# Kernel optimization log

Hardware: AMD Instinct MI355X
Metric: run time of the kernel (lower is better)

Reference implementation:

```python
import jax, jax.numpy as jnp
import numpy as np

EMB, HID, SEQ, BATCH, VOCAB, NLAYERS = 512, 512, 64, 64, 10000, 2


def setup_inputs() -> dict:
    key = jax.random.key(0)
    ks = jax.random.split(key, 8)
    u = lambda k, s: jax.random.uniform(k, s, jnp.float32, -0.1, 0.1)
    return {
        "inputs": jax.random.randint(ks[0], (SEQ, BATCH), 0, VOCAB),  # (S,B) token ids
        "hidden": jnp.zeros((NLAYERS, BATCH, HID), jnp.float32),      # init_hidden()
        "emb": u(ks[1], (VOCAB, EMB)),                                # embedding table
        "W0": u(ks[2], (HID, EMB)),  "bW0": jnp.zeros((HID,), jnp.float32),
        "W1": u(ks[3], (HID, HID)), "bW1": jnp.zeros((HID,), jnp.float32),
        "U0": u(ks[4], (HID, HID)), "bU0": jnp.zeros((HID,), jnp.float32),
        "U1": u(ks[5], (HID, HID)), "bU1": jnp.zeros((HID,), jnp.float32),
        "Wd": u(ks[6], (VOCAB, HID)), "bd": jnp.zeros((VOCAB,), jnp.float32),
    }


def reference(inputs, hidden, emb, W0, bW0, W1, bW1, U0, bU0, U1, bU1, Wd, bd):
    # Stacked 2-layer Elman RNN; dp_keep_prob=1.0 -> dropout is identity.
    x = emb[inputs]  # (S,B,E) embedding lookup for all timesteps at once

    def step(h, x_t):
        # h: (2,B,H); x_t: (B,E)
        h0 = jnp.tanh(x_t @ W0.T + bW0 + h[0] @ U0.T + bU0)   # layer 0
        h1 = jnp.tanh(h0 @ W1.T + bW1 + h[1] @ U1.T + bU1)    # layer 1
        logits = h1 @ Wd.T + bd                                # (B,V)
        return jnp.stack([h0, h1]), logits

    h_final, logits = jax.lax.scan(step, hidden, x)
    return logits, h_final  # (S,B,V), (2,B,H)
```

## Files before the change

### kernel.cpp

```cpp
#include <hip/hip_runtime.h>
#include <hip/hip_bf16.h>
#include <hip/hip_fp16.h>


typedef _Float16 f16;
typedef _Float16 f16x8 __attribute__((ext_vector_type(8)));
typedef float fvec4 __attribute__((ext_vector_type(4)));
typedef float f32x4 __attribute__((ext_vector_type(4)));
typedef unsigned int u32;
typedef u32 u32x2 __attribute__((ext_vector_type(2)));

__device__ __forceinline__ f32x4 mfma16(f16x8 a, f16x8 b, f32x4 c) {
    return __builtin_amdgcn_mfma_f32_16x16x32_f16(a, b, c, 0, 0, 0);
}

__device__ __forceinline__ f16x8 cvt_f16x8(fvec4 a, fvec4 b) {
    f16x8 r;
    r[0] = (f16)a[0]; r[1] = (f16)a[1]; r[2] = (f16)a[2]; r[3] = (f16)a[3];
    r[4] = (f16)b[0]; r[5] = (f16)b[1]; r[6] = (f16)b[2]; r[7] = (f16)b[3];
    return r;
}

__global__ void cvt_f32_f16(const float* __restrict__ src, f16* __restrict__ dst, int n8) {
    int i = blockIdx.x * 256 + threadIdx.x;
    if (i >= n8) return;
    const fvec4* p = (const fvec4*)(src + (size_t)i * 8);
    *(f16x8*)(dst + (size_t)i * 8) = cvt_f16x8(p[0], p[1]);
}

__global__ void cvt_wd(const float* __restrict__ src, f16* __restrict__ dst) {
    int i = blockIdx.x * 256 + threadIdx.x;
    if (i >= 647168) return;
    if (i < 640000) {
        const fvec4* p = (const fvec4*)(src + (size_t)i * 8);
        *(f16x8*)(dst + (size_t)i * 8) = cvt_f16x8(p[0], p[1]);
    } else {
        f16x8 z = {};
        *(f16x8*)(dst + (size_t)i * 8) = z;
    }
}

__global__ void gather_x(const int* __restrict__ toks, const float* __restrict__ emb,
                         f16* __restrict__ xb) {
    int i = blockIdx.x * 256 + threadIdx.x;
    if (i >= 262144) return;
    int row = i >> 6, seg = i & 63;
    int tok = toks[row];
    const fvec4* p = (const fvec4*)(emb + (size_t)tok * 512 + seg * 8);
    *(f16x8*)(xb + (size_t)row * 512 + seg * 8) = cvt_f16x8(p[0], p[1]);
}

template <int MODE>
__global__ __launch_bounds__(256) void gemm_bt(
    const f16* __restrict__ A, const f16* __restrict__ Bm,
    const float* __restrict__ bias1, const float* __restrict__ bias2,
    float* __restrict__ C, int N)
{
    const int tM = blockIdx.x * 128;
    const int tN = blockIdx.y * 128;
    const int tid = threadIdx.x;
    const int l = tid & 63, w = tid >> 6;
    const int wr = w >> 1, wc = w & 1;
    const int l15 = l & 15, l4 = l >> 4;

    __shared__ f16 As[128 * 40];
    __shared__ f16 Bs[128 * 40];

    f32x4 acc[4][4] = {};

    for (int ks = 0; ks < 16; ++ks) {
        const int k0 = ks * 32;
        __syncthreads();
#pragma unroll
        for (int it = 0; it < 2; ++it) {
            int c = tid + it * 256;
            int row = c >> 2, seg = c & 3;
            *(f16x8*)(&As[row * 40 + seg * 8]) =
                *(const f16x8*)(A + (size_t)(tM + row) * 512 + k0 + seg * 8);
            *(f16x8*)(&Bs[row * 40 + seg * 8]) =
                *(const f16x8*)(Bm + (size_t)(tN + row) * 512 + k0 + seg * 8);
        }
        __syncthreads();
        f16x8 af[4], bf[4];
#pragma unroll
        for (int m = 0; m < 4; ++m)
            af[m] = *(const f16x8*)(&As[(wr * 64 + m * 16 + l15) * 40 + 8 * l4]);
#pragma unroll
        for (int n = 0; n < 4; ++n)
            bf[n] = *(const f16x8*)(&Bs[(wc * 64 + n * 16 + l15) * 40 + 8 * l4]);
#pragma unroll
        for (int m = 0; m < 4; ++m)
#pragma unroll
            for (int n = 0; n < 4; ++n)
                acc[m][n] = mfma16(af[m], bf[n], acc[m][n]);
    }

    if (MODE == 0) {
#pragma unroll
        for (int n = 0; n < 4; ++n) {
            int col = tN + wc * 64 + n * 16 + l15;
            if (col >= N) continue;
            float bsum = (bias1 ? bias1[col] : 0.f) + (bias2 ? bias2[col] : 0.f);
#pragma unroll
            for (int m = 0; m < 4; ++m)
#pragma unroll
                for (int r = 0; r < 4; ++r) {
                    int row = tM + wr * 64 + m * 16 + l4 * 4 + r;
                    C[(size_t)row * N + col] = acc[m][n][r] + bsum;
                }
        }
    } else {
        const int t  = blockIdx.x * 2 + wr;
        const int wp = blockIdx.y * 2 + wc;
        const int lp_hi = (l15 >> 2) * 16;
        const int rp = l15 & 3;
#pragma unroll
        for (int n = 0; n < 4; ++n) {
            int col = tN + wc * 64 + n * 16 + l15;
            float bsum = bias1[col] + bias2[col];
#pragma unroll
            for (int m = 0; m < 4; ++m) {
#pragma unroll
                for (int r = 0; r < 4; ++r) {
                    int lanep = lp_hi + l4 * 4 + r;
                    size_t idx = ((((size_t)t * 4 + m) * 8 + wp) * 64 + lanep) * 16
                                 + n * 4 + rp;
                    C[idx] = acc[m][n][r] + bsum;
                }
            }
        }
    }
}

__global__ __launch_bounds__(512, 1) void recur_kernel(
    const float* __restrict__ A0p,
    const float* __restrict__ U,
    const float* __restrict__ h0,
    f16* __restrict__ Hh,
    float* __restrict__ outTail)
{
    const int g = blockIdx.x;
    const int tid = threadIdx.x;
    const int l = tid & 63, w = tid >> 6;
    const int l15 = l & 15, l4 = l >> 4;
    const int colbase = w * 64;

    __shared__ __align__(16) char smem[163840];
    char* hsb  = smem;
    char* ldsB = smem + 32768;

    f16x8 bf[4][12];
#pragma unroll
    for (int nt = 0; nt < 4; ++nt) {
        const float* urow = U + (size_t)(colbase + nt * 16 + l15) * 512 + 8 * l4;
#pragma unroll
        for (int kk = 0; kk < 12; ++kk) {
            const fvec4* p = (const fvec4*)(urow + kk * 32);
            bf[nt][kk] = cvt_f16x8(p[0], p[1]);
        }
#pragma unroll
        for (int kk = 12; kk < 16; ++kk) {
            const fvec4* p = (const fvec4*)(urow + kk * 32);
            *(f16x8*)(ldsB + ((w * 4 + nt) * 4 + (kk - 12)) * 1024 + l * 16) =
                cvt_f16x8(p[0], p[1]);
        }
    }
    for (int c = tid; c < 1024; c += 512) {
        int row = c >> 6, seg = c & 63;
        const fvec4* p = (const fvec4*)(h0 + (size_t)(g * 16 + row) * 512 + seg * 8);
        *(f16x8*)(hsb + row * 1024 + ((seg * 16) ^ ((row & 7) << 4))) =
            cvt_f16x8(p[0], p[1]);
    }
    __syncthreads();

    const int sw = (l15 & 7) << 4;
    const int rowbase = l15 * 1024;

    for (int t = 0; t < 64; ++t) {
        const float* ab = A0p + (((size_t)t * 4 + g) * 8 + w) * 1024 + l * 16;
        f32x4 acc[4];
#pragma unroll
        for (int nt = 0; nt < 4; ++nt) acc[nt] = *(const fvec4*)(ab + nt * 4);

        const char* hrd = hsb + (t & 1) * 16384 + rowbase;
#pragma unroll
        for (int kk = 0; kk < 12; ++kk) {
            f16x8 h = *(const f16x8*)(hrd + ((kk * 64 + l4 * 16) ^ sw));
            acc[0] = mfma16(bf[0][kk], h, acc[0]);
            acc[1] = mfma16(bf[1][kk], h, acc[1]);
            acc[2] = mfma16(bf[2][kk], h, acc[2]);
            acc[3] = mfma16(bf[3][kk], h, acc[3]);
        }
#pragma unroll
        for (int kk = 12; kk < 16; ++kk) {
            f16x8 h = *(const f16x8*)(hrd + ((kk * 64 + l4 * 16) ^ sw));
#pragma unroll
            for (int nt = 0; nt < 4; ++nt) {
                f16x8 u = *(const f16x8*)(ldsB + ((w * 4 + nt) * 4 + (kk - 12)) * 1024 + l * 16);
                acc[nt] = mfma16(u, h, acc[nt]);
            }
        }

        char* hwr = hsb + (((t & 1) ^ 1) * 16384) + rowbase;
        f16* hrow = Hh + ((size_t)t * 64 + g * 16 + l15) * 512;
#pragma unroll
        for (int nt = 0; nt < 4; ++nt) {
            f32x4 v;
#pragma unroll
            for (int r = 0; r < 4; ++r) {
                float x = acc[nt][r];
                float e = __expf(2.0f * x);
                v[r] = 1.0f - 2.0f * __builtin_amdgcn_rcpf(e + 1.0f);
            }
            f16 h0c = (f16)v[0], h1c = (f16)v[1], h2c = (f16)v[2], h3c = (f16)v[3];
            u32 p0 = ((u32)__builtin_bit_cast(unsigned short, h1c) << 16) |
                     (u32)__builtin_bit_cast(unsigned short, h0c);
            u32 p1 = ((u32)__builtin_bit_cast(unsigned short, h3c) << 16) |
                     (u32)__builtin_bit_cast(unsigned short, h2c);
            u32x2 pk; pk[0] = p0; pk[1] = p1;
            int c0 = colbase + nt * 16 + l4 * 4;
            *(u32x2*)(hwr + ((c0 * 2) ^ sw)) = pk;
            *(u32x2*)(hrow + c0) = pk;
            if (t == 63)
                *(f32x4*)(outTail + (size_t)(g * 16 + l15) * 512 + c0) = v;
        }
        __syncthreads();
    }
}

extern "C" void kernel_launch(void* const* d_in, const int* in_sizes, int n_in,
                              void* d_out, int out_size, void* d_ws, size_t ws_size,
                              hipStream_t stream) {
    const int*   toks   = (const int*)d_in[0];
    const float* hidden = (const float*)d_in[1];
    const float* emb    = (const float*)d_in[2];
    const float* W0  = (const float*)d_in[3];
    const float* bW0 = (const float*)d_in[4];
    const float* W1  = (const float*)d_in[5];
    const float* bW1 = (const float*)d_in[6];
    const float* U0  = (const float*)d_in[7];
    const float* bU0 = (const float*)d_in[8];
    const float* U1  = (const float*)d_in[9];
    const float* bU1 = (const float*)d_in[10];
    const float* Wd  = (const float*)d_in[11];
    const float* bd  = (const float*)d_in[12];
    float* out = (float*)d_out;

    char* ws = (char*)d_ws;
    f16*   W0h  = (f16*)(ws + 0);
    f16*   W1h  = (f16*)(ws + 524288);
    f16*   Wdh  = (f16*)(ws + 1048576);
    f16*   Xb   = (f16*)(ws + 11403264);
    f16*   H0h  = (f16*)(ws + 15597568);
    f16*   H1h  = (f16*)(ws + 19791872);
    float* A0   = (float*)(ws + 23986176);
    float* B1   = (float*)(ws + 32374784);

    cvt_f32_f16<<<128, 256, 0, stream>>>(W0, W0h, 32768);
    cvt_f32_f16<<<128, 256, 0, stream>>>(W1, W1h, 32768);
    cvt_wd<<<2528, 256, 0, stream>>>(Wd, Wdh);
    gather_x<<<1024, 256, 0, stream>>>(toks, emb, Xb);

    gemm_bt<1><<<dim3(32, 4), 256, 0, stream>>>(Xb, W0h, bW0, bU0, A0, 512);
    recur_kernel<<<4, 512, 0, stream>>>(A0, U0, hidden, H0h, out + 40960000);
    gemm_bt<1><<<dim3(32, 4), 256, 0, stream>>>(H0h, W1h, bW1, bU1, B1, 512);
    recur_kernel<<<4, 512, 0, stream>>>(B1, U1, hidden + 32768, H1h,
                                        out + 40960000 + 32768);
    gemm_bt<0><<<dim3(32, 79), 256, 0, stream>>>(H1h, Wdh, bd, nullptr, out, 10000);
}
```

Baseline: 505.1 us.

## Fuse both RNN layers and the layer-1 input GEMM into one pipelined persistent kernel

Replaces the two sequential recurrence kernels and the intermediate W1 GEMM with a single 24-block persistent kernel. Layer-0 blocks publish each timestep's hidden state and bump a flag. Sixteen producer blocks wait on that flag and compute the W1 projection for that step, then layer-1 blocks consume it behind their own flags. The goal is to overlap layer 0 and layer 1 across timesteps and drop two launches plus the serial W1 GEMM. The cost is spin-wait synchronisation through global atomics and fences on every step, and it relies on all 24 blocks being co-resident.

```diff
diff --git a/kernel.cpp b/kernel.cpp
--- a/kernel.cpp
+++ b/kernel.cpp
@@ -9,6 +9,8 @@
 typedef float f32x4 __attribute__((ext_vector_type(4)));
 typedef unsigned int u32;
 typedef u32 u32x2 __attribute__((ext_vector_type(2)));
+
+#define AGENT __HIP_MEMORY_SCOPE_AGENT
 
 __device__ __forceinline__ f32x4 mfma16(f16x8 a, f16x8 b, f32x4 c) {
     return __builtin_amdgcn_mfma_f32_16x16x32_f16(a, b, c, 0, 0, 0);
@@ -48,6 +50,11 @@
     int tok = toks[row];
     const fvec4* p = (const fvec4*)(emb + (size_t)tok * 512 + seg * 8);
     *(f16x8*)(xb + (size_t)row * 512 + seg * 8) = cvt_f16x8(p[0], p[1]);
+}
+
+__global__ void zero_u32(u32* p, int n) {
+    int i = blockIdx.x * 256 + threadIdx.x;
+    if (i < n) p[i] = 0;
 }
 
 template <int MODE>
@@ -132,20 +139,16 @@
     }
 }
 
-__global__ __launch_bounds__(512, 1) void recur_kernel(
-    const float* __restrict__ A0p,
-    const float* __restrict__ U,
-    const float* __restrict__ h0,
-    f16* __restrict__ Hh,
-    float* __restrict__ outTail)
+template <int ROLE>
+__device__ __forceinline__ void recur_role(
+    char* smem, int g, const float* Ainp, const float* U, const float* h0,
+    f16* hp0, f16* Hh, float* outTail, u32* flag0, u32* flag1)
 {
-    const int g = blockIdx.x;
     const int tid = threadIdx.x;
     const int l = tid & 63, w = tid >> 6;
     const int l15 = l & 15, l4 = l >> 4;
     const int colbase = w * 64;
 
-    __shared__ __align__(16) char smem[163840];
     char* hsb  = smem;
     char* ldsB = smem + 32768;
 
@@ -177,7 +180,18 @@
     const int rowbase = l15 * 1024;
 
     for (int t = 0; t < 64; ++t) {
-        const float* ab = A0p + (((size_t)t * 4 + g) * 8 + w) * 1024 + l * 16;
+        if (ROLE == 1) {
+            if (tid == 0) {
+#pragma unroll
+                for (int q = 0; q < 4; ++q)
+                    while (__hip_atomic_load(&flag1[g * 4 + q], __ATOMIC_ACQUIRE,
+                                             AGENT) < (u32)(t + 1))
+                        __builtin_amdgcn_s_sleep(1);
+            }
+            __syncthreads();
+        }
+
+        const float* ab = Ainp + (((size_t)t * 4 + g) * 8 + w) * 1024 + l * 16;
         f32x4 acc[4];
 #pragma unroll
         for (int nt = 0; nt < 4; ++nt) acc[nt] = *(const fvec4*)(ab + nt * 4);
@@ -202,7 +216,9 @@
         }
 
         char* hwr = hsb + (((t & 1) ^ 1) * 16384) + rowbase;
-        f16* hrow = Hh + ((size_t)t * 64 + g * 16 + l15) * 512;
+        f16* hrow = (ROLE == 0)
+            ? hp0 + ((size_t)(g * 64 + t)) * 8192 + l15 * 512
+            : Hh + ((size_t)t * 64 + g * 16 + l15) * 512;
 #pragma unroll
         for (int nt = 0; nt < 4; ++nt) {
             f32x4 v;
@@ -224,7 +240,86 @@
             if (t == 63)
                 *(f32x4*)(outTail + (size_t)(g * 16 + l15) * 512 + c0) = v;
         }
+        if (ROLE == 0) __threadfence();
         __syncthreads();
+        if (ROLE == 0 && tid == 0)
+            __hip_atomic_store(&flag0[g], (u32)(t + 1), __ATOMIC_RELEASE, AGENT);
+    }
+}
+
+__global__ __launch_bounds__(512) void mega_recur(
+    const float* __restrict__ A0p, float* __restrict__ A1p,
+    const float* __restrict__ U0, const float* __restrict__ U1,
+    const float* __restrict__ W1,
+    const float* __restrict__ bW1, const float* __restrict__ bU1,
+    const float* __restrict__ hidden,
+    f16* __restrict__ hp0, f16* __restrict__ H1h,
+    float* __restrict__ outT, u32* __restrict__ flags)
+{
+    __shared__ __align__(16) char smem[163840];
+    u32* flag0 = flags;
+    u32* flag1 = flags + 4;
+    const int bid = blockIdx.x;
+
+    if (bid < 4) {
+        recur_role<0>(smem, bid, A0p, U0, hidden, hp0, nullptr,
+                      outT, flag0, flag1);
+    } else if (bid < 20) {
+        const int g = (bid - 4) >> 2, q = (bid - 4) & 3;
+        const int tid = threadIdx.x;
+        const int l = tid & 63, wv = tid >> 6;
+        const int l15 = l & 15, l4 = l >> 4;
+        const int sw = (l15 & 7) << 4;
+
+        f16x8 wf[16];
+        {
+            const float* wrow = W1 + (size_t)(q * 128 + wv * 16 + l15) * 512 + 8 * l4;
+#pragma unroll
+            for (int kk = 0; kk < 16; ++kk) {
+                const fvec4* p = (const fvec4*)(wrow + kk * 32);
+                wf[kk] = cvt_f16x8(p[0], p[1]);
+            }
+        }
+        const int colb = q * 128 + wv * 16 + l4 * 4;
+        fvec4 bsum = *(const fvec4*)(bW1 + colb);
+        bsum += *(const fvec4*)(bU1 + colb);
+
+        const int wdst = q * 2 + (wv >> 2);
+        const int ntd  = wv & 3;
+
+        for (int t = 0; t < 64; ++t) {
+            if (tid == 0) {
+                while (__hip_atomic_load(&flag0[g], __ATOMIC_ACQUIRE, AGENT) <
+                       (u32)(t + 1))
+                    __builtin_amdgcn_s_sleep(1);
+            }
+            __syncthreads();
+            const f16* hsrc = hp0 + ((size_t)(g * 64 + t)) * 8192;
+            char* hb = smem + (t & 1) * 16384;
+            for (int c = tid; c < 1024; c += 512) {
+                int row = c >> 6, seg = c & 63;
+                *(f16x8*)(hb + row * 1024 + ((seg * 16) ^ ((row & 7) << 4))) =
+                    *(const f16x8*)(hsrc + row * 512 + seg * 8);
+            }
+            __syncthreads();
+
+            f32x4 acc = bsum;
+            const char* hrd = hb + l15 * 1024;
+#pragma unroll
+            for (int kk = 0; kk < 16; ++kk) {
+                f16x8 h = *(const f16x8*)(hrd + ((kk * 64 + l4 * 16) ^ sw));
+                acc = mfma16(wf[kk], h, acc);
+            }
+            float* dst = A1p + ((((size_t)t * 4 + g) * 8 + wdst) * 64 + l) * 16 + ntd * 4;
+            *(f32x4*)dst = acc;
+            __threadfence();
+            __syncthreads();
+            if (tid == 0)
+                __hip_atomic_fetch_add(&flag1[g * 4 + q], 1u, __ATOMIC_RELEASE, AGENT);
+        }
+    } else {
+        recur_role<1>(smem, bid - 20, A1p, U1, hidden + 32768, nullptr, H1h,
+                      outT + 32768, flag0, flag1);
     }
 }
 
@@ -248,23 +343,21 @@
 
     char* ws = (char*)d_ws;
     f16*   W0h  = (f16*)(ws + 0);
-    f16*   W1h  = (f16*)(ws + 524288);
     f16*   Wdh  = (f16*)(ws + 1048576);
     f16*   Xb   = (f16*)(ws + 11403264);
-    f16*   H0h  = (f16*)(ws + 15597568);
+    f16*   hp0  = (f16*)(ws + 15597568);
     f16*   H1h  = (f16*)(ws + 19791872);
     float* A0   = (float*)(ws + 23986176);
-    float* B1   = (float*)(ws + 32374784);
+    float* A1p  = (float*)(ws + 32374784);
+    u32*   flags= (u32*)(ws + 40763392);
 
     cvt_f32_f16<<<128, 256, 0, stream>>>(W0, W0h, 32768);
-    cvt_f32_f16<<<128, 256, 0, stream>>>(W1, W1h, 32768);
     cvt_wd<<<2528, 256, 0, stream>>>(Wd, Wdh);
     gather_x<<<1024, 256, 0, stream>>>(toks, emb, Xb);
+    zero_u32<<<1, 256, 0, stream>>>(flags, 20);
 
     gemm_bt<1><<<dim3(32, 4), 256, 0, stream>>>(Xb, W0h, bW0, bU0, A0, 512);
-    recur_kernel<<<4, 512, 0, stream>>>(A0, U0, hidden, H0h, out + 40960000);
-    gemm_bt<1><<<dim3(32, 4), 256, 0, stream>>>(H0h, W1h, bW1, bU1, B1, 512);
-    recur_kernel<<<4, 512, 0, stream>>>(B1, U1, hidden + 32768, H1h,
-                                        out + 40960000 + 32768);
+    mega_recur<<<24, 512, 0, stream>>>(A0, A1p, U0, U1, W1, bW1, bU1, hidden,
+                                       hp0, H1h, out + 40960000, flags);
     gemm_bt<0><<<dim3(32, 79), 256, 0, stream>>>(H1h, Wdh, bd, nullptr, out, 10000);
 }
```

Measured after the change: 649.1 us. 28.5% more time.

## Split each recurrence batch group across four workgroups with global flag synchronization

Applied to the files above, without the earlier changes.

The recurrent kernel now spreads each 16-row batch group's 512 hidden columns over four workgroups instead of one. Each wave holds the full K of its 16 U columns in registers, and the per-step LDS spill of the U tile is removed. After each timestep the new hidden slice goes to a global double buffer, and an acquire/release flag counter per quarter lets all four workgroups wait for each other before the next step. This quadruples the CUs working on the serial chain and cuts per-wave MFMA work per step. In exchange, every step pays a global-memory round trip and a spin-wait across workgroups, and progress depends on all 16 active blocks being resident at once.

```diff
diff --git a/kernel.cpp b/kernel.cpp
--- a/kernel.cpp
+++ b/kernel.cpp
@@ -9,6 +9,8 @@
 typedef float f32x4 __attribute__((ext_vector_type(4)));
 typedef unsigned int u32;
 typedef u32 u32x2 __attribute__((ext_vector_type(2)));
+
+#define AGENT __HIP_MEMORY_SCOPE_AGENT
 
 __device__ __forceinline__ f32x4 mfma16(f16x8 a, f16x8 b, f32x4 c) {
     return __builtin_amdgcn_mfma_f32_16x16x32_f16(a, b, c, 0, 0, 0);
@@ -48,6 +50,11 @@
     int tok = toks[row];
     const fvec4* p = (const fvec4*)(emb + (size_t)tok * 512 + seg * 8);
     *(f16x8*)(xb + (size_t)row * 512 + seg * 8) = cvt_f16x8(p[0], p[1]);
+}
+
+__global__ void zero_u32(u32* p, int n) {
+    int i = blockIdx.x * 256 + threadIdx.x;
+    if (i < n) p[i] = 0;
 }
 
 template <int MODE>
@@ -132,99 +139,104 @@
     }
 }
 
-__global__ __launch_bounds__(512, 1) void recur_kernel(
-    const float* __restrict__ A0p,
+__global__ __launch_bounds__(512) void recur_split(
+    const float* __restrict__ Ainp,
     const float* __restrict__ U,
     const float* __restrict__ h0,
     f16* __restrict__ Hh,
-    float* __restrict__ outTail)
+    float* __restrict__ outTail,
+    f16* __restrict__ hx,
+    u32* __restrict__ flags)
 {
-    const int g = blockIdx.x;
+    const int bid = blockIdx.x;
+    const int g = bid & 7;
+    if (g >= 4) return;
+    const int q = bid >> 3;
     const int tid = threadIdx.x;
-    const int l = tid & 63, w = tid >> 6;
+    const int l = tid & 63, wv = tid >> 6;
     const int l15 = l & 15, l4 = l >> 4;
-    const int colbase = w * 64;
-
-    __shared__ __align__(16) char smem[163840];
-    char* hsb  = smem;
-    char* ldsB = smem + 32768;
-
-    f16x8 bf[4][12];
-#pragma unroll
-    for (int nt = 0; nt < 4; ++nt) {
-        const float* urow = U + (size_t)(colbase + nt * 16 + l15) * 512 + 8 * l4;
-#pragma unroll
-        for (int kk = 0; kk < 12; ++kk) {
+    const int cs = q * 128 + wv * 16;
+
+    __shared__ __align__(16) char smem[32768];
+
+    f16x8 wf[16];
+    {
+        const float* urow = U + (size_t)(cs + l15) * 512 + 8 * l4;
+#pragma unroll
+        for (int kk = 0; kk < 16; ++kk) {
             const fvec4* p = (const fvec4*)(urow + kk * 32);
-            bf[nt][kk] = cvt_f16x8(p[0], p[1]);
-        }
-#pragma unroll
-        for (int kk = 12; kk < 16; ++kk) {
-            const fvec4* p = (const fvec4*)(urow + kk * 32);
-            *(f16x8*)(ldsB + ((w * 4 + nt) * 4 + (kk - 12)) * 1024 + l * 16) =
-                cvt_f16x8(p[0], p[1]);
-        }
-    }
-    for (int c = tid; c < 1024; c += 512) {
-        int row = c >> 6, seg = c & 63;
-        const fvec4* p = (const fvec4*)(h0 + (size_t)(g * 16 + row) * 512 + seg * 8);
-        *(f16x8*)(hsb + row * 1024 + ((seg * 16) ^ ((row & 7) << 4))) =
-            cvt_f16x8(p[0], p[1]);
-    }
-    __syncthreads();
-
+            wf[kk] = cvt_f16x8(p[0], p[1]);
+        }
+    }
+
+    u32* flg = flags + g * 4;
+    f16* hxg = hx + (size_t)g * 16384;
     const int sw = (l15 & 7) << 4;
-    const int rowbase = l15 * 1024;
 
     for (int t = 0; t < 64; ++t) {
-        const float* ab = A0p + (((size_t)t * 4 + g) * 8 + w) * 1024 + l * 16;
-        f32x4 acc[4];
-#pragma unroll
-        for (int nt = 0; nt < 4; ++nt) acc[nt] = *(const fvec4*)(ab + nt * 4);
-
-        const char* hrd = hsb + (t & 1) * 16384 + rowbase;
-#pragma unroll
-        for (int kk = 0; kk < 12; ++kk) {
+        if (t > 0) {
+            if (tid == 0) {
+#pragma unroll
+                for (int qq = 0; qq < 4; ++qq)
+                    while (__hip_atomic_load(&flg[qq], __ATOMIC_ACQUIRE, AGENT) <
+                           (u32)t)
+                        __builtin_amdgcn_s_sleep(1);
+            }
+            __syncthreads();
+        }
+        char* hb = smem + (t & 1) * 16384;
+        if (t == 0) {
+            for (int c = tid; c < 1024; c += 512) {
+                int row = c >> 6, seg = c & 63;
+                const fvec4* p =
+                    (const fvec4*)(h0 + (size_t)(g * 16 + row) * 512 + seg * 8);
+                *(f16x8*)(hb + row * 1024 + ((seg * 16) ^ ((row & 7) << 4))) =
+                    cvt_f16x8(p[0], p[1]);
+            }
+        } else {
+            const f16* hsrc = hxg + ((t - 1) & 1) * 8192;
+            for (int c = tid; c < 1024; c += 512) {
+                int row = c >> 6, seg = c & 63;
+                *(f16x8*)(hb + row * 1024 + ((seg * 16) ^ ((row & 7) << 4))) =
+                    *(const f16x8*)(hsrc + row * 512 + seg * 8);
+            }
+        }
+        __syncthreads();
+
+        const float* ab = Ainp +
+            (((size_t)t * 4 + g) * 8 + q * 2 + (wv >> 2)) * 1024 + l * 16 +
+            (wv & 3) * 4;
+        f32x4 acc = *(const f32x4*)ab;
+
+        const char* hrd = hb + l15 * 1024;
+#pragma unroll
+        for (int kk = 0; kk < 16; ++kk) {
             f16x8 h = *(const f16x8*)(hrd + ((kk * 64 + l4 * 16) ^ sw));
-            acc[0] = mfma16(bf[0][kk], h, acc[0]);
-            acc[1] = mfma16(bf[1][kk], h, acc[1]);
-            acc[2] = mfma16(bf[2][kk], h, acc[2]);
-            acc[3] = mfma16(bf[3][kk], h, acc[3]);
-        }
-#pragma unroll
-        for (int kk = 12; kk < 16; ++kk) {
-            f16x8 h = *(const f16x8*)(hrd + ((kk * 64 + l4 * 16) ^ sw));
-#pragma unroll
-            for (int nt = 0; nt < 4; ++nt) {
-                f16x8 u = *(const f16x8*)(ldsB + ((w * 4 + nt) * 4 + (kk - 12)) * 1024 + l * 16);
-                acc[nt] = mfma16(u, h, acc[nt]);
-            }
-        }
-
-        char* hwr = hsb + (((t & 1) ^ 1) * 16384) + rowbase;
-        f16* hrow = Hh + ((size_t)t * 64 + g * 16 + l15) * 512;
-#pragma unroll
-        for (int nt = 0; nt < 4; ++nt) {
-            f32x4 v;
-#pragma unroll
-            for (int r = 0; r < 4; ++r) {
-                float x = acc[nt][r];
-                float e = __expf(2.0f * x);
-                v[r] = 1.0f - 2.0f * __builtin_amdgcn_rcpf(e + 1.0f);
-            }
-            f16 h0c = (f16)v[0], h1c = (f16)v[1], h2c = (f16)v[2], h3c = (f16)v[3];
-            u32 p0 = ((u32)__builtin_bit_cast(unsigned short, h1c) << 16) |
-                     (u32)__builtin_bit_cast(unsigned short, h0c);
-            u32 p1 = ((u32)__builtin_bit_cast(unsigned short, h3c) << 16) |
-                     (u32)__builtin_bit_cast(unsigned short, h2c);
-            u32x2 pk; pk[0] = p0; pk[1] = p1;
-            int c0 = colbase + nt * 16 + l4 * 4;
-            *(u32x2*)(hwr + ((c0 * 2) ^ sw)) = pk;
-            *(u32x2*)(hrow + c0) = pk;
-            if (t == 63)
-                *(f32x4*)(outTail + (size_t)(g * 16 + l15) * 512 + c0) = v;
-        }
-        __syncthreads();
+            acc = mfma16(wf[kk], h, acc);
+        }
+
+        f32x4 v;
+#pragma unroll
+        for (int r = 0; r < 4; ++r) {
+            float e = __expf(2.0f * acc[r]);
+            v[r] = 1.0f - 2.0f * __builtin_amdgcn_rcpf(e + 1.0f);
+        }
+        f16 c0f = (f16)v[0], c1f = (f16)v[1], c2f = (f16)v[2], c3f = (f16)v[3];
+        u32 p0 = ((u32)__builtin_bit_cast(unsigned short, c1f) << 16) |
+                 (u32)__builtin_bit_cast(unsigned short, c0f);
+        u32 p1 = ((u32)__builtin_bit_cast(unsigned short, c3f) << 16) |
+                 (u32)__builtin_bit_cast(unsigned short, c2f);
+        u32x2 pk; pk[0] = p0; pk[1] = p1;
+        const int c0 = cs + l4 * 4;
+        *(u32x2*)(hxg + (t & 1) * 8192 + l15 * 512 + c0) = pk;
+        *(u32x2*)(Hh + ((size_t)t * 64 + g * 16 + l15) * 512 + c0) = pk;
+        if (t == 63)
+            *(f32x4*)(outTail + (size_t)(g * 16 + l15) * 512 + c0) = v;
+
+        __threadfence();
+        __syncthreads();
+        if (tid == 0)
+            __hip_atomic_store(&flg[q], (u32)(t + 1), __ATOMIC_RELEASE, AGENT);
     }
 }
 
@@ -255,16 +267,20 @@
     f16*   H1h  = (f16*)(ws + 19791872);
     float* A0   = (float*)(ws + 23986176);
     float* B1   = (float*)(ws + 32374784);
+    f16*   hx   = (f16*)(ws + 40763392);
+    u32*   flags= (u32*)(ws + 40894464);
 
     cvt_f32_f16<<<128, 256, 0, stream>>>(W0, W0h, 32768);
     cvt_f32_f16<<<128, 256, 0, stream>>>(W1, W1h, 32768);
     cvt_wd<<<2528, 256, 0, stream>>>(Wd, Wdh);
     gather_x<<<1024, 256, 0, stream>>>(toks, emb, Xb);
+    zero_u32<<<1, 256, 0, stream>>>(flags, 32);
 
     gemm_bt<1><<<dim3(32, 4), 256, 0, stream>>>(Xb, W0h, bW0, bU0, A0, 512);
-    recur_kernel<<<4, 512, 0, stream>>>(A0, U0, hidden, H0h, out + 40960000);
+    recur_split<<<32, 512, 0, stream>>>(A0, U0, hidden, H0h,
+                                        out + 40960000, hx, flags);
     gemm_bt<1><<<dim3(32, 4), 256, 0, stream>>>(H0h, W1h, bW1, bU1, B1, 512);
-    recur_kernel<<<4, 512, 0, stream>>>(B1, U1, hidden + 32768, H1h,
-                                        out + 40960000 + 32768);
+    recur_split<<<32, 512, 0, stream>>>(B1, U1, hidden + 32768, H1h,
+                                        out + 40960000 + 32768, hx, flags + 16);
     gemm_bt<0><<<dim3(32, 79), 256, 0, stream>>>(H1h, Wdh, bd, nullptr, out, 10000);
 }
```

New measurement: 1.302 ms. 2.58x slower.
